# Optimization experiments

Hardware: AMD Instinct MI355X
Metric: run time of the kernel (lower is better)

The kernel has to match this reference:

```python
import jax, jax.numpy as jnp
import numpy as np
from jax import lax

L = 2      # num_layers
H = 256    # behavior_size (forced by split(256) in decoder)
K = 128    # input_size / output_size (pose dim)
B = 512    # batch == start_size == output_length (len(pose_sequence))
T = 64     # encoder / teacher-forced sequence length


def gru_cell(x, h, Wih, Whh, bih, bhh):
    # PyTorch GRU cell math. x: [B,in], h: [B,H]
    gi = x @ Wih.T + bih            # [B, 3H]
    gh = h @ Whh.T + bhh            # [B, 3H]
    i_r, i_z, i_n = jnp.split(gi, 3, axis=-1)
    h_r, h_z, h_n = jnp.split(gh, 3, axis=-1)
    r = jax.nn.sigmoid(i_r + h_r)
    z = jax.nn.sigmoid(i_z + h_z)
    n = jnp.tanh(i_n + r * h_n)
    return (1.0 - z) * n + z * h


def _stack_step(params):
    # one timestep through a stacked GRU; params: list of (Wih,Whh,bih,bhh)
    def step(h, x_t):  # h: [L,B,H], x_t: [B,in]
        inp = x_t
        hs = []
        for l, (Wih, Whh, bih, bhh) in enumerate(params):
            hl = gru_cell(inp, h[l], Wih, Whh, bih, bhh)
            hs.append(hl)
            inp = hl
        return jnp.stack(hs), inp  # new hidden, top-layer output
    return step


def _forward(pose_sequence,
             enc_Wih0, enc_Whh0, enc_bih0, enc_bhh0,
             enc_Wih1, enc_Whh1, enc_bih1, enc_bhh1,
             dec_Wih0, dec_Whh0, dec_bih0, dec_bhh0,
             dec_Wih1, dec_Whh1, dec_bih1, dec_bhh1,
             out_W, out_b):
    enc_p = [(enc_Wih0, enc_Whh0, enc_bih0, enc_bhh0),
             (enc_Wih1, enc_Whh1, enc_bih1, enc_bhh1)]
    dec_p = [(dec_Wih0, dec_Whh0, dec_bih0, dec_bhh0),
             (dec_Wih1, dec_Whh1, dec_bih1, dec_bhh1)]
    bs, t, _ = pose_sequence.shape
    dt = pose_sequence.dtype

    # ---- Encoder: stacked GRU over time, keep final hidden [L,B,H] ----
    h0 = jnp.zeros((L, bs, H), dtype=dt)
    enc_step = _stack_step(enc_p)
    h_enc, _ = lax.scan(lambda h, x: (enc_step(h, x)[0], None), h0,
                        jnp.swapaxes(pose_sequence, 0, 1))
    # behavior_encoding = cat(hidden.split(1,0), -1) [B, L*H]; decoder
    # re-stacks via split(256) -> identical hidden, so use h_enc directly.

    # ---- Decoder ----
    start_condition = pose_sequence[:B]          # start_size == batch
    output_length = pose_sequence.shape[0]       # len(pose_sequence)
    dec_step = _stack_step(dec_p)

    def proj(top):  # output_layer
        return top @ out_W.T + out_b

    # phase 1: teacher-forced over the start_condition timesteps
    def step1(h, x_t):
        new_h, top = dec_step(h, x_t)
        return new_h, proj(top)
    h1, outs1 = lax.scan(step1, h_enc, jnp.swapaxes(start_condition, 0, 1))
    out_last = outs1[-1]                         # [B,K]

    n2 = output_length - t
    def step2(carry, _):
        out, h = carry
        new_h, top = dec_step(h, out)
        new_out = proj(top)
        return (new_out, new_h), new_out
    _, outs2 = lax.scan(step2, (out_last, h1), None, length=n2)

    outs = jnp.concatenate([outs1, outs2], axis=0)  # [T_total, B, K]
    return jnp.swapaxes(outs, 0, 1)                 # [B, T_total, K]


def setup_inputs() -> dict:
    key = jax.random.key(0)
    ks = jax.random.split(key, 20)
    s = 1.0 / np.sqrt(H)  # torch GRU/Linear init scale
    u = lambda k, shape: jax.random.uniform(k, shape, jnp.float32, -s, s)
    inp = {
        'pose_sequence': jax.random.normal(ks[0], (B, T, K), jnp.float32),
        # encoder GRU (layer0 in=K, layer1 in=H)
        'enc_Wih0': u(ks[1], (3 * H, K)), 'enc_Whh0': u(ks[2], (3 * H, H)),
        'enc_bih0': u(ks[3], (3 * H,)),  'enc_bhh0': u(ks[4], (3 * H,)),
        'enc_Wih1': u(ks[5], (3 * H, H)), 'enc_Whh1': u(ks[6], (3 * H, H)),
        'enc_bih1': u(ks[7], (3 * H,)),  'enc_bhh1': u(ks[8], (3 * H,)),
        # decoder GRU
        'dec_Wih0': u(ks[9], (3 * H, K)), 'dec_Whh0': u(ks[10], (3 * H, H)),
        'dec_bih0': u(ks[11], (3 * H,)), 'dec_bhh0': u(ks[12], (3 * H,)),
        'dec_Wih1': u(ks[13], (3 * H, H)), 'dec_Whh1': u(ks[14], (3 * H, H)),
        'dec_bih1': u(ks[15], (3 * H,)), 'dec_bhh1': u(ks[16], (3 * H,)),
        # output projection H -> K
        'out_W': u(ks[17], (K, H)), 'out_b': u(ks[18], (K,)),
    }
    return inp


def reference(pose_sequence,
              enc_Wih0, enc_Whh0, enc_bih0, enc_bhh0,
              enc_Wih1, enc_Whh1, enc_bih1, enc_bhh1,
              dec_Wih0, dec_Whh0, dec_bih0, dec_bhh0,
              dec_Wih1, dec_Whh1, dec_bih1, dec_bhh1,
              out_W, out_b):
    return _forward(pose_sequence,
                    enc_Wih0, enc_Whh0, enc_bih0, enc_bhh0,
                    enc_Wih1, enc_Whh1, enc_bih1, enc_bhh1,
                    dec_Wih0, dec_Whh0, dec_bih0, dec_bhh0,
                    dec_Wih1, dec_Whh1, dec_bih1, dec_bhh1,
                    out_W, out_b)
```

## Files before the change

kernel.cpp:

```cpp
#include <hip/hip_runtime.h>
#include <cstddef>
#include <cstdint>


typedef __attribute__((ext_vector_type(8))) _Float16 half8v;
typedef __attribute__((ext_vector_type(4))) float float4v;
typedef __attribute__((ext_vector_type(4))) unsigned uint4v;

static const size_t OFF_H0A = 0;
static const size_t OFF_H1A = 131072;
static const size_t OFF_H0B = 262144;
static const size_t OFF_H1B = 393216;
static const size_t OFF_WF  = 524288;
static const size_t OFF_BF  = OFF_WF + 196608;
static const size_t OFF_CTR = OFF_BF + 1024;
static const size_t OFF_CLM = OFF_CTR + 2048;

#define SIGF(x) (1.0f / (1.0f + __expf(-(x))))
#define MFMA16F __builtin_amdgcn_mfma_f32_16x16x32_f16
#define MM2(C, W, BH, BL) \
    C = MFMA16F(W, BH, C, 0, 0, 0); \
    C = MFMA16F(W, BL, C, 0, 0, 0);

__device__ __forceinline__ unsigned pack_h(float x) {
    _Float16 h = (_Float16)x;
    _Float16 l = (_Float16)(x - (float)h);
    unsigned short uh = __builtin_bit_cast(unsigned short, h);
    unsigned short ul = __builtin_bit_cast(unsigned short, l);
    return (unsigned)uh | ((unsigned)ul << 16);
}

__device__ __forceinline__ void ld32_sc0(const void* p, uint4v& a, uint4v& b) {
    asm volatile("global_load_dwordx4 %0, %2, off sc0\n\t"
                 "global_load_dwordx4 %1, %2, off offset:16 sc0\n\t"
                 "s_waitcnt vmcnt(0)"
                 : "=v"(a), "=v"(b) : "v"(p) : "memory");
}

__global__ void fuse_wb(const float* __restrict__ Wih0, const float* __restrict__ oW,
                        const float* __restrict__ ob, const float* __restrict__ bih0,
                        float* __restrict__ Wf, float* __restrict__ bf) {
    int idx = blockIdx.x * 256 + threadIdx.x;
    int r = idx >> 8, h = idx & 255;
    const float* wr = Wih0 + (size_t)r * 128;
    float a = 0.f;
    for (int k = 0; k < 128; ++k) a = fmaf(wr[k], oW[(size_t)k * 256 + h], a);
    Wf[idx] = a;
    if (h == 0) {
        float b = 0.f;
        for (int k = 0; k < 128; ++k) b = fmaf(wr[k], ob[k], b);
        bf[r] = b + bih0[r];
    }
}

__global__ __launch_bounds__(512, 1)
void behav_main(
    const float* __restrict__ pose,
    const float* __restrict__ eW0i, const float* __restrict__ eW0h,
    const float* __restrict__ eb0i, const float* __restrict__ eb0h,
    const float* __restrict__ eW1i, const float* __restrict__ eW1h,
    const float* __restrict__ eb1i, const float* __restrict__ eb1h,
    const float* __restrict__ dW0i, const float* __restrict__ dW0h,
    const float* __restrict__ db0i, const float* __restrict__ db0h,
    const float* __restrict__ dW1i, const float* __restrict__ dW1h,
    const float* __restrict__ db1i, const float* __restrict__ db1h,
    const float* __restrict__ oW, const float* __restrict__ ob,
    float* __restrict__ out,
    float* h0a, float* h0b, float* h1a, float* h1b,
    const float* __restrict__ Wf, const float* __restrict__ bf,
    unsigned* ctrs, unsigned* clm)
{
    __shared__ _Float16 Ah[16][256], Al[16][256], Bh[16][256], Bl[16][256];
    __shared__ float Gt[24 * 288];
    __shared__ float Hp0[16][32], Hp1[16][32];
    __shared__ unsigned s_lin;

    const int tid = threadIdx.x;
    const int lane = tid & 63;
    const int w = tid >> 6;

    if (tid == 0) {
        unsigned xcc;
        asm volatile("s_getreg_b32 %0, hwreg(HW_REG_XCC_ID)" : "=s"(xcc));
        xcc &= 7u;
        unsigned pos = __hip_atomic_fetch_add(&clm[xcc], 1u,
                           __ATOMIC_RELAXED, __HIP_MEMORY_SCOPE_AGENT);
        s_lin = (xcc << 5) | (pos & 31u);
    }
    __syncthreads();
    const unsigned lin = s_lin;
    const int c = (int)(lin >> 3);
    const int uwg = (int)(lin & 7);
    const int s0 = c << 4, j0 = uwg << 5;
    unsigned* ctr = ctrs + (c << 6);
    unsigned epoch = 0;

    unsigned* h0pk[2] = { (unsigned*)h0a, (unsigned*)h0b };
    unsigned* h1pk[2] = { (unsigned*)h1a, (unsigned*)h1b };
    int pp = 0;

    const float4v FZ = {0.f, 0.f, 0.f, 0.f};
    const float obv = ((tid & 31) < 16) ? ob[(uwg << 4) + (tid & 31)] : 0.f;

    auto cbar = [&]() {
        __syncthreads();
        ++epoch;
        if (tid == 0) {
            __hip_atomic_fetch_add(ctr, 1u, __ATOMIC_RELAXED, __HIP_MEMORY_SCOPE_AGENT);
            unsigned tgt = epoch * 8u;
            while (__hip_atomic_load(ctr, __ATOMIC_RELAXED, __HIP_MEMORY_SCOPE_AGENT) < tgt)
                __builtin_amdgcn_s_sleep(1);
        }
        __syncthreads();
    };

    auto ldfrag = [&](const float* M, int ldm, int row0, int col0, half8v& wv) {
        const float* p = M + (size_t)(row0 + (lane & 15)) * ldm + col0 + ((lane >> 4) << 3);
        float4 a = *(const float4*)p;
        float4 b = *(const float4*)(p + 4);
        float vv[8] = {a.x, a.y, a.z, a.w, b.x, b.y, b.z, b.w};
        #pragma unroll
        for (int i = 0; i < 8; ++i) wv[i] = (_Float16)vv[i];
    };
    auto rdS = [&](const _Float16 (*arr)[256], int kloc) -> half8v {
        int s = lane & 15, o = lane >> 4;
        int phys = ((kloc << 2) + o) ^ (s & 7);
        return *(const half8v*)&arr[s][phys << 3];
    };
    auto rdX = [&](int t, int loc, half8v& bh, half8v& bl) {
        const float* p = pose + (size_t)(s0 + (lane & 15)) * 8192 + (size_t)t * 128
                         + (loc << 5) + ((lane >> 4) << 3);
        float4 a = *(const float4*)p;
        float4 b = *(const float4*)(p + 4);
        float vv[8] = {a.x, a.y, a.z, a.w, b.x, b.y, b.z, b.w};
        #pragma unroll
        for (int i = 0; i < 8; ++i) {
            _Float16 h = (_Float16)vv[i];
            bh[i] = h;
            bl[i] = (_Float16)(vv[i] - (float)h);
        }
    };
    auto stage = [&](_Float16 (*ha)[256], _Float16 (*la)[256], const unsigned* src) {
        int s = tid >> 5, cc = tid & 31;
        uint4v a, b;
        ld32_sc0((const void*)(src + (size_t)(s0 + s) * 256 + (cc << 3)), a, b);
        unsigned u[8] = {a.x, a.y, a.z, a.w, b.x, b.y, b.z, b.w};
        half8v hv, lv;
        #pragma unroll
        for (int i = 0; i < 8; ++i) {
            hv[i] = __builtin_bit_cast(_Float16, (unsigned short)(u[i] & 0xFFFF));
            lv[i] = __builtin_bit_cast(_Float16, (unsigned short)(u[i] >> 16));
        }
        int phys = cc ^ (s & 7);
        *(half8v*)&ha[s][phys << 3] = hv;
        *(half8v*)&la[s][phys << 3] = lv;
    };
    auto gdump = [&](int slot, float4v a) {
        int col = lane & 15, ro = (lane >> 4) << 2;
        float* b = &Gt[slot * 288 + ro * 18 + col];
        b[0] = a.x; b[18] = a.y; b[36] = a.z; b[54] = a.w;
    };
    auto gtr = [&](int slot, int r16, int s) -> float {
        return Gt[slot * 288 + r16 * 18 + s];
    };

    half8v WA[16], WB[8], WC[4];
    float b0r, b0z, b0ni, b0nh, b1r, b1z, b1ni, b1nh;

    auto load_era = [&](const float* W0i, bool x128, const float* W0h,
                        const float* W1i, const float* W1h) {
        if (w < 6) {
            const int rb1 = ((w >> 1) << 8) + j0 + ((w & 1) << 4);
            if (x128) {
                #pragma unroll
                for (int cc = 0; cc < 4; ++cc) ldfrag(W0i, 128, rb1, cc << 5, WA[cc]);
            } else {
                #pragma unroll
                for (int cc = 0; cc < 8; ++cc) ldfrag(W0i, 256, rb1, cc << 5, WA[cc]);
            }
            #pragma unroll
            for (int cc = 0; cc < 8; ++cc) ldfrag(W0h, 256, rb1, cc << 5, WA[8 + cc]);
            const int t2 = w >> 1;
            const int rb2 = ((t2 >> 1) << 8) + j0 + ((t2 & 1) << 4);
            const int kb = (w & 1) << 2;
            #pragma unroll
            for (int cc = 0; cc < 4; ++cc) ldfrag(W1h, 256, rb2, (kb + cc) << 5, WC[cc]);
            if (w < 4) {
                #pragma unroll
                for (int cc = 0; cc < 8; ++cc) ldfrag(W1i, 256, rb1, cc << 5, WB[cc]);
            } else {
                const int rb3 = 512 + j0 + ((w - 4) << 4);
                #pragma unroll
                for (int cc = 0; cc < 4; ++cc) ldfrag(W1i, 256, rb3, cc << 5, WB[cc]);
            }
        } else {
            #pragma unroll
            for (int j = 0; j < 3; ++j) {
                const int hh = 6 + (w - 6) * 3 + j;
                const int t2 = hh >> 1;
                const int rb2 = ((t2 >> 1) << 8) + j0 + ((t2 & 1) << 4);
                const int kb = (hh & 1) << 2;
                #pragma unroll
                for (int cc = 0; cc < 4; ++cc)
                    ldfrag(W1h, 256, rb2, (kb + cc) << 5, WA[4 * j + cc]);
            }
            #pragma unroll
            for (int cc = 0; cc < 4; ++cc)
                ldfrag(oW, 256, uwg << 4, (((w - 6) << 2) + cc) << 5, WA[12 + cc]);
            const int rb3 = 512 + j0 + ((w - 6) << 4);
            #pragma unroll
            for (int cc = 0; cc < 4; ++cc) ldfrag(W1i, 256, rb3, (4 + cc) << 5, WB[cc]);
        }
    };
    auto ldb0 = [&](const float* bi, const float* bhh) {
        int jj = j0 + (tid & 31);
        b0r = bi[jj] + bhh[jj]; b0z = bi[256 + jj] + bhh[256 + jj];
        b0ni = bi[512 + jj]; b0nh = bhh[512 + jj];
    };
    auto ldb1 = [&](const float* bi, const float* bhh) {
        int jj = j0 + (tid & 31);
        b1r = bi[jj] + bhh[jj]; b1z = bi[256 + jj] + bhh[256 + jj];
        b1ni = bi[512 + jj]; b1nh = bhh[512 + jj];
    };

    auto W1_fn = [&](int t, bool xs, bool pj) {
        if (w < 6) {
            float4v accI = FZ, accH = FZ;
            if (xs) {
                #pragma unroll
                for (int cc = 0; cc < 4; ++cc) {
                    half8v bh, bl; rdX(t, cc, bh, bl);
                    MM2(accI, WA[cc], bh, bl);
                }
            } else {
                #pragma unroll
                for (int cc = 0; cc < 8; ++cc) {
                    half8v bh = rdS(Ah, cc), bl = rdS(Al, cc);
                    MM2(accI, WA[cc], bh, bl);
                }
            }
            if (w >= 4) {
                #pragma unroll
                for (int cc = 0; cc < 8; ++cc) {
                    half8v bh = rdS(Bh, cc), bl = rdS(Bl, cc);
                    MM2(accH, WA[8 + cc], bh, bl);
                }
                gdump(w, accI);
                gdump(22 + (w - 4), accH);
            } else {
                #pragma unroll
                for (int cc = 0; cc < 8; ++cc) {
                    half8v bh = rdS(Bh, cc), bl = rdS(Bl, cc);
                    MM2(accI, WA[8 + cc], bh, bl);
                }
                gdump(w, accI);
            }
            float4v accP = FZ;
            const int kb = (w & 1) << 2;
            #pragma unroll
            for (int cc = 0; cc < 4; ++cc) {
                half8v bh = rdS(Ah, kb + cc), bl = rdS(Al, kb + cc);
                MM2(accP, WC[cc], bh, bl);
            }
            gdump(6 + w, accP);
        } else {
            #pragma unroll
            for (int j = 0; j < 3; ++j) {
                const int hh = 6 + (w - 6) * 3 + j;
                const int kb = (hh & 1) << 2;
                float4v accP = FZ;
                #pragma unroll
                for (int cc = 0; cc < 4; ++cc) {
                    half8v bh = rdS(Ah, kb + cc), bl = rdS(Al, kb + cc);
                    MM2(accP, WA[4 * j + cc], bh, bl);
                }
                gdump(6 + hh, accP);
            }
            if (pj) {
                float4v accJ = FZ;
                const int cb = (w - 6) << 2;
                #pragma unroll
                for (int cc = 0; cc < 4; ++cc) {
                    half8v bh = rdS(Ah, cb + cc), bl = rdS(Al, cb + cc);
                    MM2(accJ, WA[12 + cc], bh, bl);
                }
                gdump(18 + (w - 6), accJ);
            }
        }
    };
    auto W2_fn = [&]() {
        if (w < 4) {
            float4v acc = FZ;
            #pragma unroll
            for (int cc = 0; cc < 8; ++cc) {
                half8v bh = rdS(Bh, cc), bl = rdS(Bl, cc);
                MM2(acc, WB[cc], bh, bl);
            }
            gdump(w, acc);
        } else {
            float4v acc = FZ;
            const int kb = (w >= 6) ? 4 : 0;
            #pragma unroll
            for (int cc = 0; cc < 4; ++cc) {
                half8v bh = rdS(Bh, kb + cc), bl = rdS(Bl, kb + cc);
                MM2(acc, WB[cc], bh, bl);
            }
            const int sl = (w == 4) ? 4 : (w == 5) ? 20 : (w == 6) ? 5 : 21;
            gdump(sl, acc);
        }
    };
    auto epi1 = [&](unsigned* pongpk) {
        int s = tid >> 5, ul = tid & 31, t2 = ul >> 4, r16 = ul & 15;
        float r = SIGF(gtr(t2, r16, s) + b0r);
        float z = SIGF(gtr(2 + t2, r16, s) + b0z);
        float n = tanhf(gtr(4 + t2, r16, s) + b0ni + r * (gtr(22 + t2, r16, s) + b0nh));
        float h = (1.f - z) * n + z * Hp0[s][ul];
        Hp0[s][ul] = h;
        pongpk[(size_t)(s0 + s) * 256 + j0 + ul] = pack_h(h);
    };
    auto epi2 = [&](unsigned* pongpk) {
        int s = tid >> 5, ul = tid & 31, t2 = ul >> 4, r16 = ul & 15;
        float r = SIGF(gtr(t2, r16, s) + gtr(6 + (t2 << 1), r16, s)
                       + gtr(7 + (t2 << 1), r16, s) + b1r);
        float z = SIGF(gtr(2 + t2, r16, s) + gtr(10 + (t2 << 1), r16, s)
                       + gtr(11 + (t2 << 1), r16, s) + b1z);
        int nia = t2 ? 20 : 4, nib = t2 ? 21 : 5;
        float ni = gtr(nia, r16, s) + gtr(nib, r16, s);
        float nh = gtr(14 + (t2 << 1), r16, s) + gtr(15 + (t2 << 1), r16, s);
        float n = tanhf(ni + b1ni + r * (nh + b1nh));
        float h = (1.f - z) * n + z * Hp1[s][ul];
        Hp1[s][ul] = h;
        pongpk[(size_t)(s0 + s) * 256 + j0 + ul] = pack_h(h);
    };
    auto epi_proj = [&](int tq) {
        int s = tid >> 5, ul = tid & 31;
        if (ul < 16) {
            float v = gtr(18, ul, s) + gtr(19, ul, s) + obv;
            out[(size_t)(s0 + s) * 65536 + (size_t)tq * 128 + (uwg << 4) + ul] = v;
        }
    };

    auto step = [&](int t, bool xs, bool pj) {
        W1_fn(t, xs, pj);
        __syncthreads();
        epi1(h0pk[pp ^ 1]);
        cbar();
        stage(Bh, Bl, h0pk[pp ^ 1]);
        if (pj) epi_proj(t - 1);
        __syncthreads();
        W2_fn();
        __syncthreads();
        epi2(h1pk[pp ^ 1]);
        cbar();
        stage(Ah, Al, h1pk[pp ^ 1]);
        __syncthreads();
        pp ^= 1;
    };

    {
        int s = tid >> 5, cc = tid & 31;
        half8v z;
        #pragma unroll
        for (int i = 0; i < 8; ++i) z[i] = (_Float16)0.f;
        *(half8v*)&Ah[s][cc << 3] = z;
        *(half8v*)&Al[s][cc << 3] = z;
        *(half8v*)&Bh[s][cc << 3] = z;
        *(half8v*)&Bl[s][cc << 3] = z;
        Hp0[s][cc] = 0.f;
        Hp1[s][cc] = 0.f;
    }
    __syncthreads();

    load_era(eW0i, true, eW0h, eW1i, eW1h);
    ldb0(eb0i, eb0h); ldb1(eb1i, eb1h);
    for (int t = 0; t < 64; ++t) step(t, true, false);

    load_era(dW0i, true, dW0h, dW1i, dW1h);
    ldb0(db0i, db0h); ldb1(db1i, db1h);
    step(0, true, false);
    for (int t = 1; t < 64; ++t) step(t, true, true);

    if (w < 6) {
        const int rb1 = ((w >> 1) << 8) + j0 + ((w & 1) << 4);
        #pragma unroll
        for (int cc = 0; cc < 8; ++cc) ldfrag(Wf, 256, rb1, cc << 5, WA[cc]);
    }
    {
        int jj = j0 + (tid & 31);
        b0r = bf[jj] + db0h[jj];
        b0z = bf[256 + jj] + db0h[256 + jj];
        b0ni = bf[512 + jj];
        b0nh = db0h[512 + jj];
    }
    for (int t = 64; t < 512; ++t) step(t, false, true);

    if (w >= 6) {
        float4v accJ = FZ;
        const int cb = (w - 6) << 2;
        #pragma unroll
        for (int cc = 0; cc < 4; ++cc) {
            half8v bh = rdS(Ah, cb + cc), bl = rdS(Al, cb + cc);
            MM2(accJ, WA[12 + cc], bh, bl);
        }
        gdump(18 + (w - 6), accJ);
    }
    __syncthreads();
    epi_proj(511);
}

extern "C" void kernel_launch(void* const* d_in, const int* in_sizes, int n_in,
                              void* d_out, int out_size, void* d_ws, size_t ws_size,
                              hipStream_t stream) {
    (void)in_sizes; (void)n_in; (void)out_size; (void)ws_size;

    const float* pose = (const float*)d_in[0];
    const float* eW0i = (const float*)d_in[1];
    const float* eW0h = (const float*)d_in[2];
    const float* eb0i = (const float*)d_in[3];
    const float* eb0h = (const float*)d_in[4];
    const float* eW1i = (const float*)d_in[5];
    const float* eW1h = (const float*)d_in[6];
    const float* eb1i = (const float*)d_in[7];
    const float* eb1h = (const float*)d_in[8];
    const float* dW0i = (const float*)d_in[9];
    const float* dW0h = (const float*)d_in[10];
    const float* db0i = (const float*)d_in[11];
    const float* db0h = (const float*)d_in[12];
    const float* dW1i = (const float*)d_in[13];
    const float* dW1h = (const float*)d_in[14];
    const float* db1i = (const float*)d_in[15];
    const float* db1h = (const float*)d_in[16];
    const float* oW   = (const float*)d_in[17];
    const float* ob   = (const float*)d_in[18];

    float* ws = (float*)d_ws;
    float* h0a = ws + OFF_H0A;
    float* h0b = ws + OFF_H0B;
    float* h1a = ws + OFF_H1A;
    float* h1b = ws + OFF_H1B;
    float* Wf  = ws + OFF_WF;
    float* bf  = ws + OFF_BF;
    unsigned* ctrs = (unsigned*)(ws + OFF_CTR);
    unsigned* clm  = (unsigned*)(ws + OFF_CLM);
    float* outf = (float*)d_out;

    hipMemsetAsync((void*)ctrs, 0, (2048 + 64) * sizeof(unsigned), stream);

    fuse_wb<<<dim3(768), dim3(256), 0, stream>>>(dW0i, oW, ob, db0i, Wf, bf);

    void* kargs[] = {
        (void*)&pose,
        (void*)&eW0i, (void*)&eW0h, (void*)&eb0i, (void*)&eb0h,
        (void*)&eW1i, (void*)&eW1h, (void*)&eb1i, (void*)&eb1h,
        (void*)&dW0i, (void*)&dW0h, (void*)&db0i, (void*)&db0h,
        (void*)&dW1i, (void*)&dW1h, (void*)&db1i, (void*)&db1h,
        (void*)&oW, (void*)&ob,
        (void*)&outf,
        (void*)&h0a, (void*)&h0b, (void*)&h1a, (void*)&h1b,
        (void*)&Wf, (void*)&bf,
        (void*)&ctrs, (void*)&clm
    };
    hipLaunchCooperativeKernel((const void*)behav_main, dim3(256), dim3(512),
                               kargs, 0, stream);
}
```

Measured before the change: 3.197 ms.

## Split grid barrier into arrive/wait and overlap independent matmuls in the wait

Splits the cross-workgroup barrier into an arrive and a wait. Work that does not depend on peers' new hidden state now runs between the two: the layer-1 input projections and output projection, plus the next step's layer-0 recurrent matmul on the already-staged layer-0 hidden. These are stored in extra scratch slots and added back in the next epilogue. This hides barrier latency on the serial recurrence, but adds shared memory and boundary-step conditions (first and last step) that must be handled correctly.

```diff
diff --git a/kernel.cpp b/kernel.cpp
--- a/kernel.cpp
+++ b/kernel.cpp
@@ -71,7 +71,7 @@
     unsigned* ctrs, unsigned* clm)
 {
     __shared__ _Float16 Ah[16][256], Al[16][256], Bh[16][256], Bl[16][256];
-    __shared__ float Gt[24 * 288];
+    __shared__ float Gt[28 * 288];
     __shared__ float Hp0[16][32], Hp1[16][32];
     __shared__ unsigned s_lin;
 
@@ -102,11 +102,14 @@
     const float4v FZ = {0.f, 0.f, 0.f, 0.f};
     const float obv = ((tid & 31) < 16) ? ob[(uwg << 4) + (tid & 31)] : 0.f;
 
-    auto cbar = [&]() {
+    auto arrive = [&]() {
         __syncthreads();
         ++epoch;
+        if (tid == 0)
+            __hip_atomic_fetch_add(ctr, 1u, __ATOMIC_RELAXED, __HIP_MEMORY_SCOPE_AGENT);
+    };
+    auto waitf = [&]() {
         if (tid == 0) {
-            __hip_atomic_fetch_add(ctr, 1u, __ATOMIC_RELAXED, __HIP_MEMORY_SCOPE_AGENT);
             unsigned tgt = epoch * 8u;
             while (__hip_atomic_load(ctr, __ATOMIC_RELAXED, __HIP_MEMORY_SCOPE_AGENT) < tgt)
                 __builtin_amdgcn_s_sleep(1);
@@ -223,23 +226,32 @@
         b1ni = bi[512 + jj]; b1nh = bhh[512 + jj];
     };
 
-    auto W1_fn = [&](int t, bool xs, bool pj) {
-        if (w < 6) {
-            float4v accI = FZ, accH = FZ;
-            if (xs) {
-                #pragma unroll
-                for (int cc = 0; cc < 4; ++cc) {
-                    half8v bh, bl; rdX(t, cc, bh, bl);
-                    MM2(accI, WA[cc], bh, bl);
+    auto phaseA = [&](int t, bool xs, bool pre) {
+        if (w >= 6) return;
+        float4v accI = FZ;
+        if (xs) {
+            #pragma unroll
+            for (int cc = 0; cc < 4; ++cc) {
+                half8v bh, bl; rdX(t, cc, bh, bl);
+                MM2(accI, WA[cc], bh, bl);
+            }
+        } else {
+            #pragma unroll
+            for (int cc = 0; cc < 8; ++cc) {
+                half8v bh = rdS(Ah, cc), bl = rdS(Al, cc);
+                MM2(accI, WA[cc], bh, bl);
+            }
+        }
+        if (!pre) {
+            if (w < 4) {
+                #pragma unroll
+                for (int cc = 0; cc < 8; ++cc) {
+                    half8v bh = rdS(Bh, cc), bl = rdS(Bl, cc);
+                    MM2(accI, WA[8 + cc], bh, bl);
                 }
+                gdump(w, accI);
             } else {
-                #pragma unroll
-                for (int cc = 0; cc < 8; ++cc) {
-                    half8v bh = rdS(Ah, cc), bl = rdS(Al, cc);
-                    MM2(accI, WA[cc], bh, bl);
-                }
-            }
-            if (w >= 4) {
+                float4v accH = FZ;
                 #pragma unroll
                 for (int cc = 0; cc < 8; ++cc) {
                     half8v bh = rdS(Bh, cc), bl = rdS(Bl, cc);
@@ -247,14 +259,23 @@
                 }
                 gdump(w, accI);
                 gdump(22 + (w - 4), accH);
-            } else {
-                #pragma unroll
-                for (int cc = 0; cc < 8; ++cc) {
-                    half8v bh = rdS(Bh, cc), bl = rdS(Bl, cc);
-                    MM2(accI, WA[8 + cc], bh, bl);
-                }
-                gdump(w, accI);
-            }
+            }
+        } else {
+            gdump(w, accI);
+        }
+    };
+    auto shadow2 = [&]() {
+        if (w >= 6) return;
+        float4v accH = FZ;
+        #pragma unroll
+        for (int cc = 0; cc < 8; ++cc) {
+            half8v bh = rdS(Bh, cc), bl = rdS(Bl, cc);
+            MM2(accH, WA[8 + cc], bh, bl);
+        }
+        gdump((w < 4) ? (24 + w) : (22 + (w - 4)), accH);
+    };
+    auto shadow1 = [&](bool pj) {
+        if (w < 6) {
             float4v accP = FZ;
             const int kb = (w & 1) << 2;
             #pragma unroll
@@ -264,31 +285,38 @@
             }
             gdump(6 + w, accP);
         } else {
-            #pragma unroll
-            for (int j = 0; j < 3; ++j) {
-                const int hh = 6 + (w - 6) * 3 + j;
-                const int kb = (hh & 1) << 2;
-                float4v accP = FZ;
-                #pragma unroll
-                for (int cc = 0; cc < 4; ++cc) {
-                    half8v bh = rdS(Ah, kb + cc), bl = rdS(Al, kb + cc);
-                    MM2(accP, WA[4 * j + cc], bh, bl);
+            float4v A0 = FZ, A1 = FZ, A2 = FZ, AJ = FZ;
+            const bool w6 = (w == 6);
+            #pragma unroll
+            for (int cc = 0; cc < 4; ++cc) {
+                half8v bh = rdS(Ah, cc), bl = rdS(Al, cc);
+                if (w6) {
+                    MM2(A0, WA[cc], bh, bl);
+                    MM2(A2, WA[8 + cc], bh, bl);
+                    if (pj) { MM2(AJ, WA[12 + cc], bh, bl); }
+                } else {
+                    MM2(A1, WA[4 + cc], bh, bl);
                 }
-                gdump(6 + hh, accP);
-            }
-            if (pj) {
-                float4v accJ = FZ;
-                const int cb = (w - 6) << 2;
-                #pragma unroll
-                for (int cc = 0; cc < 4; ++cc) {
-                    half8v bh = rdS(Ah, cb + cc), bl = rdS(Al, cb + cc);
-                    MM2(accJ, WA[12 + cc], bh, bl);
+            }
+            #pragma unroll
+            for (int cc = 0; cc < 4; ++cc) {
+                half8v bh = rdS(Ah, 4 + cc), bl = rdS(Al, 4 + cc);
+                if (w6) {
+                    MM2(A1, WA[4 + cc], bh, bl);
+                } else {
+                    MM2(A0, WA[cc], bh, bl);
+                    MM2(A2, WA[8 + cc], bh, bl);
+                    if (pj) { MM2(AJ, WA[12 + cc], bh, bl); }
                 }
-                gdump(18 + (w - 6), accJ);
-            }
-        }
-    };
-    auto W2_fn = [&]() {
+            }
+            const int base = 12 + (w - 6) * 3;
+            gdump(base + 0, A0);
+            gdump(base + 1, A1);
+            gdump(base + 2, A2);
+            if (pj) gdump(18 + (w - 6), AJ);
+        }
+    };
+    auto phaseB = [&]() {
         if (w < 4) {
             float4v acc = FZ;
             #pragma unroll
@@ -309,10 +337,13 @@
             gdump(sl, acc);
         }
     };
-    auto epi1 = [&](unsigned* pongpk) {
+    auto epi1 = [&](unsigned* pongpk, bool pre) {
         int s = tid >> 5, ul = tid & 31, t2 = ul >> 4, r16 = ul & 15;
-        float r = SIGF(gtr(t2, r16, s) + b0r);
-        float z = SIGF(gtr(2 + t2, r16, s) + b0z);
+        float gr = gtr(t2, r16, s);
+        float gz = gtr(2 + t2, r16, s);
+        if (pre) { gr += gtr(24 + t2, r16, s); gz += gtr(26 + t2, r16, s); }
+        float r = SIGF(gr + b0r);
+        float z = SIGF(gz + b0z);
         float n = tanhf(gtr(4 + t2, r16, s) + b0ni + r * (gtr(22 + t2, r16, s) + b0nh));
         float h = (1.f - z) * n + z * Hp0[s][ul];
         Hp0[s][ul] = h;
@@ -340,18 +371,22 @@
         }
     };
 
-    auto step = [&](int t, bool xs, bool pj) {
-        W1_fn(t, xs, pj);
-        __syncthreads();
-        epi1(h0pk[pp ^ 1]);
-        cbar();
+    auto step = [&](int t, bool xs, bool pj, bool pre, bool sh2) {
+        phaseA(t, xs, pre);
+        __syncthreads();
+        epi1(h0pk[pp ^ 1], pre);
+        arrive();
+        shadow1(pj);
+        waitf();
         stage(Bh, Bl, h0pk[pp ^ 1]);
         if (pj) epi_proj(t - 1);
         __syncthreads();
-        W2_fn();
+        phaseB();
         __syncthreads();
         epi2(h1pk[pp ^ 1]);
-        cbar();
+        arrive();
+        if (sh2) shadow2();
+        waitf();
         stage(Ah, Al, h1pk[pp ^ 1]);
         __syncthreads();
         pp ^= 1;
@@ -373,26 +408,25 @@
 
     load_era(eW0i, true, eW0h, eW1i, eW1h);
     ldb0(eb0i, eb0h); ldb1(eb1i, eb1h);
-    for (int t = 0; t < 64; ++t) step(t, true, false);
+    for (int t = 0; t < 64; ++t) step(t, true, false, t > 0, t < 63);
 
     load_era(dW0i, true, dW0h, dW1i, dW1h);
     ldb0(db0i, db0h); ldb1(db1i, db1h);
-    step(0, true, false);
-    for (int t = 1; t < 64; ++t) step(t, true, true);
-
-    if (w < 6) {
-        const int rb1 = ((w >> 1) << 8) + j0 + ((w & 1) << 4);
-        #pragma unroll
-        for (int cc = 0; cc < 8; ++cc) ldfrag(Wf, 256, rb1, cc << 5, WA[cc]);
+    for (int t = 0; t < 512; ++t) {
+        if (t == 64) {
+            if (w < 6) {
+                const int rb1 = ((w >> 1) << 8) + j0 + ((w & 1) << 4);
+                #pragma unroll
+                for (int cc = 0; cc < 8; ++cc) ldfrag(Wf, 256, rb1, cc << 5, WA[cc]);
+            }
+            int jj = j0 + (tid & 31);
+            b0r = bf[jj] + db0h[jj];
+            b0z = bf[256 + jj] + db0h[256 + jj];
+            b0ni = bf[512 + jj];
+            b0nh = db0h[512 + jj];
+        }
+        step(t, t < 64, t >= 1, t > 0, t < 511);
     }
-    {
-        int jj = j0 + (tid & 31);
-        b0r = bf[jj] + db0h[jj];
-        b0z = bf[256 + jj] + db0h[256 + jj];
-        b0ni = bf[512 + jj];
-        b0nh = db0h[512 + jj];
-    }
-    for (int t = 64; t < 512; ++t) step(t, false, true);
 
     if (w >= 6) {
         float4v accJ = FZ;
```

Measured after the change: 2.602 ms, median of 2. -18.6%, faster.
